# Optimization experiments

Hardware: AMD Instinct MI355X
Metric: run time of the kernel (lower is better)

The kernel has to match this reference:

```python
import jax, jax.numpy as jnp
import numpy as np

EPS = 1e-7          # K.epsilon()
START_TEMP = 10.0
MIN_TEMP = 0.1
ALPHA = 0.99999


def setup_inputs() -> dict:
    key = jax.random.key(0)
    k1, k2, k3, k4 = jax.random.split(key, 4)
    batch, n_feat, bins, out_dim = 4096, 20000, 64, 256
    X = jax.random.normal(k1, (batch, n_feat), dtype=jnp.float32)
    u = jax.random.normal(k2, (n_feat, bins), dtype=jnp.float32)
    # keras 'uniform' initializer ~ U(-0.05, 0.05)
    tinyW = jax.random.uniform(k3, (bins, out_dim), minval=-0.05, maxval=0.05, dtype=jnp.float32)
    uniform = jax.random.uniform(k4, (out_dim, n_feat), minval=EPS, maxval=1.0, dtype=jnp.float32)
    return {"X": X, "u": u, "tinyW": tinyW, "uniform": uniform}


def reference(X, u, tinyW, uniform):
    # al = softmax(u @ tinyW) over output_dim axis, then transpose -> (D, N)
    al = jax.nn.softmax(jnp.dot(u, tinyW), axis=-1).T            # (D, N)
    logits = jnp.log(10.0 * jnp.clip(al, EPS, 0.9999999))        # (D, N)
    gumbel = -jnp.log(-jnp.log(uniform))                          # (D, N)
    temp = jnp.maximum(MIN_TEMP, START_TEMP * ALPHA)              # one K.update step
    samples = jax.nn.softmax((logits + gumbel) / temp, axis=-1)   # (D, N)

    D, N = samples.shape

    # Greedy global-argmax with row/column suppression (inference path).
    # Each of the D iterations picks the global max of p, marks dl[x, y] = 1,
    # then masks row x and column y with -1 (as the numpy loop does).
    def step(carry, _):
        p, dl = carry
        ind = jnp.argmax(p)            # flat argmax over D*N
        x = ind // N
        y = ind % N
        dl = dl.at[x, y].set(1.0)
        p = p.at[x, :].set(-1.0)
        p = p.at[:, y].set(-1.0)
        return (p, dl), None

    (_, dl), _ = jax.lax.scan(step, (samples, jnp.zeros_like(samples)), None, length=D)
    # After D iterations each row of dl has exactly one 1, so
    # one_hot(argmax(dl, axis=-1)) == dl; selections = dl in inference mode.
    Y = jnp.dot(X, dl.T)               # (batch, D)
    return Y
```

## Files before the change

kernel.cpp:

```cpp
#include <hip/hip_runtime.h>
#include <cmath>
#include <cfloat>
#include <climits>

#define NFEAT 20000
#define DDIM 256
#define KDIM 64
#define NSEG 313
#define SEGP 320

__device__ __forceinline__ double z_post(double Lraw, float uu) {
  double L = fmin(fmax(Lraw, -16.118095650958320), -1.0000000500000034e-7);
  double g = -log(-log((double)uu));
  return (2.302585092994045684 + L + g) / 9.9999;
}

__device__ __forceinline__ double compute_z(
    const float* __restrict__ u, const float* __restrict__ W,
    const float* __restrict__ unif, const double* __restrict__ lseN,
    int dd, int n) {
  double acc = 0.0;
  const float* ur = u + (size_t)n * KDIM;
#pragma unroll 8
  for (int k = 0; k < KDIM; ++k)
    acc = fma((double)ur[k], (double)W[k * DDIM + dd], acc);
  double Lraw = acc - lseN[n];
  return z_post(Lraw, unif[(size_t)dd * NFEAT + n]);
}

__global__ __launch_bounds__(256) void k_seg(
    const float* __restrict__ u, const float* __restrict__ W,
    const float* __restrict__ unif, double* __restrict__ lseN,
    double* __restrict__ segVal, double* __restrict__ segSum,
    int* __restrict__ segCol) {
  const int s = blockIdx.x;
  const int n0 = s * 64;
  const int nv = min(64, NFEAT - n0);
  const int d = threadIdx.x;
  const int lane = d & 63, w = d >> 6;

  __shared__ __align__(16) float ut[64 * 64];
  __shared__ float unT[32 * 256];
  __shared__ double ssum[4][8];
  __shared__ double logZs[8];

  for (int i = d; i < 64 * 64; i += 256) {
    int r = i >> 6;
    ut[i] = (r < nv) ? u[(size_t)(n0 + r) * KDIM + (i & 63)] : 0.f;
  }
  float wcol[64];
#pragma unroll
  for (int k = 0; k < KDIM; ++k) wcol[k] = W[k * DDIM + d];

  double ssl = 0.0;
  double segm = -INFINITY;
  int segc = -1;

  for (int half = 0; half < 2; ++half) {
    const int hn0 = half * 32;
    if (hn0 >= nv) break;
    const int hnv = min(32, nv - hn0);
    __syncthreads();
    for (int q = 0; q < hnv; q += 4) {
      const float4 t =
          *(const float4*)(unif + (size_t)d * NFEAT + n0 + hn0 + q);
      unT[(q + 0) * 256 + d] = t.x;
      unT[(q + 1) * 256 + d] = t.y;
      unT[(q + 2) * 256 + d] = t.z;
      unT[(q + 3) * 256 + d] = t.w;
    }
    __syncthreads();

    for (int b0 = hn0; b0 < hn0 + hnv; b0 += 8) {
      double acc[8];
#pragma unroll
      for (int i = 0; i < 8; ++i) acc[i] = 0.0;
#pragma unroll
      for (int k4 = 0; k4 < 16; ++k4) {
        const int kb = k4 * 4;
        const double w0 = (double)wcol[kb + 0], w1 = (double)wcol[kb + 1];
        const double w2 = (double)wcol[kb + 2], w3 = (double)wcol[kb + 3];
#pragma unroll
        for (int i = 0; i < 8; ++i) {
          const float4 uv = *(const float4*)&ut[(b0 + i) * 64 + kb];
          acc[i] = fma((double)uv.x, w0, acc[i]);
          acc[i] = fma((double)uv.y, w1, acc[i]);
          acc[i] = fma((double)uv.z, w2, acc[i]);
          acc[i] = fma((double)uv.w, w3, acc[i]);
        }
      }
      double sl[8];
#pragma unroll
      for (int i = 0; i < 8; ++i) sl[i] = exp(acc[i]);
#pragma unroll
      for (int off = 1; off < 64; off <<= 1)
#pragma unroll
        for (int i = 0; i < 8; ++i) sl[i] += __shfl_xor(sl[i], off, 64);
      if (lane == 0)
#pragma unroll
        for (int i = 0; i < 8; ++i) ssum[w][i] = sl[i];
      __syncthreads();
      if (d < 8) {
        double tot = ssum[0][d] + ssum[1][d] + ssum[2][d] + ssum[3][d];
        double lz = log(tot);
        logZs[d] = lz;
        lseN[n0 + b0 + d] = lz;
      }
      __syncthreads();
#pragma unroll 2
      for (int i = 0; i < 8; ++i) {
        const int n = n0 + b0 + i;
        const double zz =
            z_post(acc[i] - logZs[i], unT[(b0 + i - hn0) * 256 + d]);
        ssl += exp(zz);
        if (zz > segm) { segm = zz; segc = n; }
      }
      __syncthreads();
    }
  }
  segVal[(size_t)d * SEGP + s] = segm;
  segCol[(size_t)d * SEGP + s] = segc;
  segSum[(size_t)d * SEGP + s] = ssl;
}

__global__ __launch_bounds__(64) void k_rowstat(
    const double* __restrict__ segVal, const double* __restrict__ segSum,
    const int* __restrict__ segCol, double* __restrict__ logL,
    double* __restrict__ bestKey, int* __restrict__ bestCol) {
  const int dd = blockIdx.x, lane = threadIdx.x;
  double sum = 0.0, bv = -INFINITY;
  int bc = INT_MAX;
  for (int s = lane; s < NSEG; s += 64) {
    sum += segSum[(size_t)dd * SEGP + s];
    double v = segVal[(size_t)dd * SEGP + s];
    int c = segCol[(size_t)dd * SEGP + s];
    if (c >= 0 && (v > bv || (v == bv && c < bc))) { bv = v; bc = c; }
  }
#pragma unroll
  for (int off = 32; off > 0; off >>= 1) {
    sum += __shfl_xor(sum, off, 64);
    double ov = __shfl_xor(bv, off, 64);
    int oc = __shfl_xor(bc, off, 64);
    if (ov > bv || (ov == bv && oc < bc)) { bv = ov; bc = oc; }
  }
  if (lane == 0) {
    double lL = log(sum);
    logL[dd] = lL;
    bestKey[dd] = bv - lL;
    bestCol[dd] = bc;
  }
}

__global__ __launch_bounds__(64) void k_greedy(
    const float* __restrict__ u, const float* __restrict__ W,
    const float* __restrict__ unif, const double* __restrict__ lseN,
    double* __restrict__ segVal, int* __restrict__ segCol,
    const double* __restrict__ logL, const double* __restrict__ bestKey,
    const int* __restrict__ bestCol, int* __restrict__ sel) {
  const int lane = threadIdx.x;
  __shared__ double kk[DDIM], sk[DDIM];
  __shared__ int sr[DDIM], sc[DDIM], selL[DDIM];
  __shared__ unsigned int supp[NFEAT / 32];
  for (int i = lane; i < NFEAT / 32; i += 64) supp[i] = 0u;

  double myk[4];
  int myc[4];
#pragma unroll
  for (int i = 0; i < 4; ++i) {
    int dd = lane + 64 * i;
    myk[i] = bestKey[dd];
    myc[i] = bestCol[dd];
    kk[dd] = myk[i];
  }
  __syncthreads();
#pragma unroll
  for (int i = 0; i < 4; ++i) {
    int dd = lane + 64 * i;
    int rk = 0;
#pragma unroll 4
    for (int j = 0; j < DDIM; ++j) {
      double kj = kk[j];
      if (kj > myk[i] || (kj == myk[i] && j < dd)) ++rk;
    }
    sk[rk] = myk[i];
    sr[rk] = dd;
    sc[rk] = myc[i];
  }
  __syncthreads();

  int pos = 0;
  while (pos < DDIM) {
    const int p = pos + lane;
    const bool valid = p < DDIM;
    double kcur = 0.0;
    int r = -1, c = -1000000 - lane;
    if (valid) { kcur = sk[p]; r = sr[p]; c = sc[p]; }
    bool conf = !valid;
    if (valid) conf = (supp[c >> 5] >> (c & 31)) & 1u;
    bool dup = false;
#pragma unroll
    for (int j = 0; j < 63; ++j) {
      int cj = __shfl(c, j, 64);
      if (j < lane && cj == c) dup = true;
    }
    if (valid && dup) conf = true;
    unsigned long long bm = __ballot(conf);
    int fc = bm ? (__ffsll(bm) - 1) : 64;
    if (lane < fc) {
      selL[r] = c;
      atomicOr(&supp[c >> 5], 1u << (c & 31));
    }
    __syncthreads();
    pos += fc;
    if (fc < 64 && pos < DDIM) {
      const int rr = sr[pos];
      double pbv = -INFINITY;
      int pbc = INT_MAX;
      int stale[5];
      int scnt = 0;
#pragma unroll
      for (int i2 = 0; i2 < 5; ++i2) {
        int s2 = lane + 64 * i2;
        if (s2 < NSEG) {
          double v = segVal[(size_t)rr * SEGP + s2];
          int cc = segCol[(size_t)rr * SEGP + s2];
          if (cc >= 0) {
            if ((supp[cc >> 5] >> (cc & 31)) & 1u) stale[scnt++] = s2;
            else if (v > pbv || (v == pbv && cc < pbc)) { pbv = v; pbc = cc; }
          }
        }
      }
      unsigned long long sm2 = __ballot(scnt > 0);
      while (sm2) {
        int src = __ffsll(sm2) - 1;
        int cand = (scnt > 0) ? stale[scnt - 1] : 0;
        int s2 = __shfl(cand, src, 64);
        if (lane == src) --scnt;
        int ccol = s2 * 64 + lane;
        double zv = -INFINITY;
        if (ccol < NFEAT && !((supp[ccol >> 5] >> (ccol & 31)) & 1u))
          zv = compute_z(u, W, unif, lseN, rr, ccol);
        int zc = (zv == -INFINITY) ? INT_MAX : ccol;
#pragma unroll
        for (int off = 32; off > 0; off >>= 1) {
          double ov = __shfl_xor(zv, off, 64);
          int oc = __shfl_xor(zc, off, 64);
          if (ov > zv || (ov == zv && oc < zc)) { zv = ov; zc = oc; }
        }
        if (lane == 0) {
          segVal[(size_t)rr * SEGP + s2] = (zc == INT_MAX) ? -INFINITY : zv;
          segCol[(size_t)rr * SEGP + s2] = (zc == INT_MAX) ? -1 : zc;
        }
        if (zc != INT_MAX && (zv > pbv || (zv == pbv && zc < pbc))) {
          pbv = zv;
          pbc = zc;
        }
        sm2 = __ballot(scnt > 0);
      }
#pragma unroll
      for (int off = 32; off > 0; off >>= 1) {
        double ov = __shfl_xor(pbv, off, 64);
        int oc = __shfl_xor(pbc, off, 64);
        if (ov > pbv || (ov == pbv && oc < pbc)) { pbv = ov; pbc = oc; }
      }
      const double knew = pbv - logL[rr];
      const int cn = pbc;
      int cnt = 0;
      for (int q = pos + 1 + lane; q < DDIM; q += 64) {
        double kq = sk[q];
        int rq = sr[q];
        if (kq > knew || (kq == knew && rq < rr)) ++cnt;
      }
#pragma unroll
      for (int off = 32; off > 0; off >>= 1) cnt += __shfl_xor(cnt, off, 64);
      for (int q0 = pos + 1; q0 <= pos + cnt; q0 += 64) {
        int q = q0 + lane;
        double tk = 0.0;
        int tr = 0, tc = 0;
        bool v2 = q <= pos + cnt;
        if (v2) { tk = sk[q]; tr = sr[q]; tc = sc[q]; }
        __syncthreads();
        if (v2) { sk[q - 1] = tk; sr[q - 1] = tr; sc[q - 1] = tc; }
        __syncthreads();
      }
      if (lane == 0) { sk[pos + cnt] = knew; sr[pos + cnt] = rr; sc[pos + cnt] = cn; }
      __syncthreads();
    }
  }
#pragma unroll
  for (int i = 0; i < 4; ++i) sel[lane + 64 * i] = selL[lane + 64 * i];
}

__global__ __launch_bounds__(256) void k_gather(const float* __restrict__ X,
                                                float* out) {
  const int dd = threadIdx.x;
  const size_t b = (size_t)blockIdx.x + 1;
  const int y = __float_as_int(out[dd]);
  out[b * DDIM + dd] = X[b * NFEAT + y];
}

__global__ __launch_bounds__(256) void k_row0(const float* __restrict__ X,
                                              float* out) {
  const int dd = threadIdx.x;
  const int y = __float_as_int(out[dd]);
  const float v = X[y];
  out[dd] = v;
}

extern "C" void kernel_launch(void* const* d_in, const int* in_sizes, int n_in,
                              void* d_out, int out_size, void* d_ws,
                              size_t ws_size, hipStream_t stream) {
  (void)in_sizes; (void)n_in; (void)d_ws; (void)ws_size; (void)out_size;
  const float* X = (const float*)d_in[0];
  const float* u = (const float*)d_in[1];
  const float* W = (const float*)d_in[2];
  const float* unif = (const float*)d_in[3];

  char* ob = (char*)d_out;
  int* sel = (int*)ob;
  double* lseN = (double*)(ob + 1024);
  double* logL = (double*)(ob + 161024);
  double* bestKey = (double*)(ob + 163072);
  int* bestCol = (int*)(ob + 165120);
  double* segVal = (double*)(ob + 166144);
  double* segSum = (double*)(ob + 821504);
  int* segCol = (int*)(ob + 1476864);

  k_seg<<<NSEG, 256, 0, stream>>>(u, W, unif, lseN, segVal, segSum, segCol);
  k_rowstat<<<DDIM, 64, 0, stream>>>(segVal, segSum, segCol, logL, bestKey,
                                     bestCol);
  k_greedy<<<1, 64, 0, stream>>>(u, W, unif, lseN, segVal, segCol, logL,
                                 bestKey, bestCol, sel);
  k_gather<<<4095, 256, 0, stream>>>(X, (float*)d_out);
  k_row0<<<1, 256, 0, stream>>>(X, (float*)d_out);
}
```

Before: 669.2 us.

## Switch to log2 domain with custom exp2/log2 and halve segment size

Moves the score computation into base-2 logarithms, using hand-written double-precision polynomial exp2 and log2 in place of the library exp and log. It also pre-scales u by log2(e) in shared memory as doubles. Segments shrink from 64 to 32 columns, so there are twice as many blocks in k_seg and finer-grained stale-segment recomputation in the greedy pass. This targets transcendental cost and low occupancy (313 blocks), at the risk of tiny numerical differences that could change argmax tie-breaking, and larger per-row scans in the greedy kernel.

```diff
diff --git a/kernel.cpp b/kernel.cpp
--- a/kernel.cpp
+++ b/kernel.cpp
@@ -6,16 +6,61 @@
 #define NFEAT 20000
 #define DDIM 256
 #define KDIM 64
-#define NSEG 313
-#define SEGP 320
-
-__device__ __forceinline__ double z_post(double Lraw, float uu) {
-  double L = fmin(fmax(Lraw, -16.118095650958320), -1.0000000500000034e-7);
-  double g = -log(-log((double)uu));
-  return (2.302585092994045684 + L + g) / 9.9999;
-}
-
-__device__ __forceinline__ double compute_z(
+#define SEGN 32
+#define NSEG 625
+#define SEGP 640
+
+#define LOG2E 1.4426950408889634
+#define INVT (1.0 / 9.9999)
+#define LOG2_10 3.3219280948873623
+#define G2C 0.5287663729448976
+#define LO2 -23.253496664211536
+#define HI2 -1.4426951130237154e-7
+
+__device__ __forceinline__ double fexp2(double x) {
+  const double nd = rint(x);
+  const double y = (x - nd) * 0.6931471805599453;
+  double p = 1.0 / 3628800.0;
+  p = fma(p, y, 1.0 / 362880.0);
+  p = fma(p, y, 1.0 / 40320.0);
+  p = fma(p, y, 1.0 / 5040.0);
+  p = fma(p, y, 1.0 / 720.0);
+  p = fma(p, y, 1.0 / 120.0);
+  p = fma(p, y, 1.0 / 24.0);
+  p = fma(p, y, 1.0 / 6.0);
+  p = fma(p, y, 0.5);
+  p = fma(p, y, 1.0);
+  p = fma(p, y, 1.0);
+  const int n = (int)nd;
+  const double sc = __longlong_as_double((long long)(n + 1023) << 52);
+  return p * sc;
+}
+
+__device__ __forceinline__ double flog2(double x) {
+  const long long b = __double_as_longlong(x);
+  int e = (int)(b >> 52) - 1023;
+  double m = __longlong_as_double((b & 0xfffffffffffffLL) | 0x3ff0000000000000LL);
+  if (m > 1.4142135623730951) { m *= 0.5; e += 1; }
+  const double t = (m - 1.0) / (m + 1.0);
+  const double w = t * t;
+  double p = 1.0 / 13.0;
+  p = fma(p, w, 1.0 / 11.0);
+  p = fma(p, w, 1.0 / 9.0);
+  p = fma(p, w, 1.0 / 7.0);
+  p = fma(p, w, 1.0 / 5.0);
+  p = fma(p, w, 1.0 / 3.0);
+  p = fma(p, w, 1.0);
+  return fma((2.0 * LOG2E) * t, p, (double)e);
+}
+
+__device__ __forceinline__ double z2_post(double L2raw, float uu) {
+  const double L2 = fmin(fmax(L2raw, LO2), HI2);
+  const double t = -flog2((double)uu);
+  const double g2 = G2C - flog2(t);
+  return (LOG2_10 + L2 + g2) * INVT;
+}
+
+__device__ __forceinline__ double compute_z2(
     const float* __restrict__ u, const float* __restrict__ W,
     const float* __restrict__ unif, const double* __restrict__ lseN,
     int dd, int n) {
@@ -23,9 +68,8 @@
   const float* ur = u + (size_t)n * KDIM;
 #pragma unroll 8
   for (int k = 0; k < KDIM; ++k)
-    acc = fma((double)ur[k], (double)W[k * DDIM + dd], acc);
-  double Lraw = acc - lseN[n];
-  return z_post(Lraw, unif[(size_t)dd * NFEAT + n]);
+    acc = fma((double)ur[k] * LOG2E, (double)W[k * DDIM + dd], acc);
+  return z2_post(acc - lseN[n], unif[(size_t)dd * NFEAT + n]);
 }
 
 __global__ __launch_bounds__(256) void k_seg(
@@ -34,89 +78,78 @@
     double* __restrict__ segVal, double* __restrict__ segSum,
     int* __restrict__ segCol) {
   const int s = blockIdx.x;
-  const int n0 = s * 64;
-  const int nv = min(64, NFEAT - n0);
+  const int n0 = s * SEGN;
   const int d = threadIdx.x;
   const int lane = d & 63, w = d >> 6;
 
-  __shared__ __align__(16) float ut[64 * 64];
-  __shared__ float unT[32 * 256];
+  __shared__ __align__(16) double ut2[SEGN][KDIM];
+  __shared__ float unT[SEGN][DDIM];
   __shared__ double ssum[4][8];
-  __shared__ double logZs[8];
-
-  for (int i = d; i < 64 * 64; i += 256) {
-    int r = i >> 6;
-    ut[i] = (r < nv) ? u[(size_t)(n0 + r) * KDIM + (i & 63)] : 0.f;
-  }
-  float wcol[64];
+  __shared__ double lse2s[8];
+
+  for (int i = d; i < SEGN * KDIM; i += 256)
+    ut2[i >> 6][i & 63] =
+        (double)u[(size_t)(n0 + (i >> 6)) * KDIM + (i & 63)] * LOG2E;
+  for (int q = 0; q < SEGN; q += 4) {
+    const float4 t = *(const float4*)(unif + (size_t)d * NFEAT + n0 + q);
+    unT[q + 0][d] = t.x;
+    unT[q + 1][d] = t.y;
+    unT[q + 2][d] = t.z;
+    unT[q + 3][d] = t.w;
+  }
+  float wcol[KDIM];
 #pragma unroll
   for (int k = 0; k < KDIM; ++k) wcol[k] = W[k * DDIM + d];
+  __syncthreads();
 
   double ssl = 0.0;
   double segm = -INFINITY;
   int segc = -1;
 
-  for (int half = 0; half < 2; ++half) {
-    const int hn0 = half * 32;
-    if (hn0 >= nv) break;
-    const int hnv = min(32, nv - hn0);
+  for (int b0 = 0; b0 < SEGN; b0 += 8) {
+    double acc[8];
+#pragma unroll
+    for (int i = 0; i < 8; ++i) acc[i] = 0.0;
+#pragma unroll
+    for (int k4 = 0; k4 < 16; ++k4) {
+      const int kb = k4 * 4;
+      const double w0 = (double)wcol[kb + 0], w1 = (double)wcol[kb + 1];
+      const double w2 = (double)wcol[kb + 2], w3 = (double)wcol[kb + 3];
+#pragma unroll
+      for (int i = 0; i < 8; ++i) {
+        const double2 ua = *(const double2*)&ut2[b0 + i][kb];
+        const double2 ub = *(const double2*)&ut2[b0 + i][kb + 2];
+        acc[i] = fma(ua.x, w0, acc[i]);
+        acc[i] = fma(ua.y, w1, acc[i]);
+        acc[i] = fma(ub.x, w2, acc[i]);
+        acc[i] = fma(ub.y, w3, acc[i]);
+      }
+    }
+    double sl[8];
+#pragma unroll
+    for (int i = 0; i < 8; ++i) sl[i] = fexp2(acc[i]);
+#pragma unroll
+    for (int off = 1; off < 64; off <<= 1)
+#pragma unroll
+      for (int i = 0; i < 8; ++i) sl[i] += __shfl_xor(sl[i], off, 64);
+    if (lane == 0)
+#pragma unroll
+      for (int i = 0; i < 8; ++i) ssum[w][i] = sl[i];
     __syncthreads();
-    for (int q = 0; q < hnv; q += 4) {
-      const float4 t =
-          *(const float4*)(unif + (size_t)d * NFEAT + n0 + hn0 + q);
-      unT[(q + 0) * 256 + d] = t.x;
-      unT[(q + 1) * 256 + d] = t.y;
-      unT[(q + 2) * 256 + d] = t.z;
-      unT[(q + 3) * 256 + d] = t.w;
+    if (d < 8) {
+      const double tot = ssum[0][d] + ssum[1][d] + ssum[2][d] + ssum[3][d];
+      const double lz = flog2(tot);
+      lse2s[d] = lz;
+      lseN[n0 + b0 + d] = lz;
     }
     __syncthreads();
-
-    for (int b0 = hn0; b0 < hn0 + hnv; b0 += 8) {
-      double acc[8];
-#pragma unroll
-      for (int i = 0; i < 8; ++i) acc[i] = 0.0;
-#pragma unroll
-      for (int k4 = 0; k4 < 16; ++k4) {
-        const int kb = k4 * 4;
-        const double w0 = (double)wcol[kb + 0], w1 = (double)wcol[kb + 1];
-        const double w2 = (double)wcol[kb + 2], w3 = (double)wcol[kb + 3];
-#pragma unroll
-        for (int i = 0; i < 8; ++i) {
-          const float4 uv = *(const float4*)&ut[(b0 + i) * 64 + kb];
-          acc[i] = fma((double)uv.x, w0, acc[i]);
-          acc[i] = fma((double)uv.y, w1, acc[i]);
-          acc[i] = fma((double)uv.z, w2, acc[i]);
-          acc[i] = fma((double)uv.w, w3, acc[i]);
-        }
-      }
-      double sl[8];
-#pragma unroll
-      for (int i = 0; i < 8; ++i) sl[i] = exp(acc[i]);
-#pragma unroll
-      for (int off = 1; off < 64; off <<= 1)
-#pragma unroll
-        for (int i = 0; i < 8; ++i) sl[i] += __shfl_xor(sl[i], off, 64);
-      if (lane == 0)
-#pragma unroll
-        for (int i = 0; i < 8; ++i) ssum[w][i] = sl[i];
-      __syncthreads();
-      if (d < 8) {
-        double tot = ssum[0][d] + ssum[1][d] + ssum[2][d] + ssum[3][d];
-        double lz = log(tot);
-        logZs[d] = lz;
-        lseN[n0 + b0 + d] = lz;
-      }
-      __syncthreads();
 #pragma unroll 2
-      for (int i = 0; i < 8; ++i) {
-        const int n = n0 + b0 + i;
-        const double zz =
-            z_post(acc[i] - logZs[i], unT[(b0 + i - hn0) * 256 + d]);
-        ssl += exp(zz);
-        if (zz > segm) { segm = zz; segc = n; }
-      }
-      __syncthreads();
-    }
+    for (int i = 0; i < 8; ++i) {
+      const double z2 = z2_post(acc[i] - lse2s[i], unT[b0 + i][d]);
+      ssl += fexp2(z2);
+      if (z2 > segm) { segm = z2; segc = n0 + b0 + i; }
+    }
+    __syncthreads();
   }
   segVal[(size_t)d * SEGP + s] = segm;
   segCol[(size_t)d * SEGP + s] = segc;
@@ -144,7 +177,7 @@
     if (ov > bv || (ov == bv && oc < bc)) { bv = ov; bc = oc; }
   }
   if (lane == 0) {
-    double lL = log(sum);
+    double lL = flog2(sum);
     logL[dd] = lL;
     bestKey[dd] = bv - lL;
     bestCol[dd] = bc;
@@ -189,12 +222,11 @@
   __syncthreads();
 
   int pos = 0;
-  while (pos < DDIM) {
+  for (int guard = 0; guard < 4 * DDIM && pos < DDIM; ++guard) {
     const int p = pos + lane;
     const bool valid = p < DDIM;
-    double kcur = 0.0;
     int r = -1, c = -1000000 - lane;
-    if (valid) { kcur = sk[p]; r = sr[p]; c = sc[p]; }
+    if (valid) { r = sr[p]; c = sc[p]; }
     bool conf = !valid;
     if (valid) conf = (supp[c >> 5] >> (c & 31)) & 1u;
     bool dup = false;
@@ -216,10 +248,10 @@
       const int rr = sr[pos];
       double pbv = -INFINITY;
       int pbc = INT_MAX;
-      int stale[5];
+      int stale[10];
       int scnt = 0;
 #pragma unroll
-      for (int i2 = 0; i2 < 5; ++i2) {
+      for (int i2 = 0; i2 < 10; ++i2) {
         int s2 = lane + 64 * i2;
         if (s2 < NSEG) {
           double v = segVal[(size_t)rr * SEGP + s2];
@@ -231,15 +263,15 @@
         }
       }
       unsigned long long sm2 = __ballot(scnt > 0);
-      while (sm2) {
+      for (int g2 = 0; g2 < NSEG + 4 && sm2; ++g2) {
         int src = __ffsll(sm2) - 1;
         int cand = (scnt > 0) ? stale[scnt - 1] : 0;
         int s2 = __shfl(cand, src, 64);
         if (lane == src) --scnt;
-        int ccol = s2 * 64 + lane;
+        int ccol = s2 * SEGN + lane;
         double zv = -INFINITY;
-        if (ccol < NFEAT && !((supp[ccol >> 5] >> (ccol & 31)) & 1u))
-          zv = compute_z(u, W, unif, lseN, rr, ccol);
+        if (lane < SEGN && !((supp[ccol >> 5] >> (ccol & 31)) & 1u))
+          zv = compute_z2(u, W, unif, lseN, rr, ccol);
         int zc = (zv == -INFINITY) ? INT_MAX : ccol;
 #pragma unroll
         for (int off = 32; off > 0; off >>= 1) {
@@ -323,8 +355,8 @@
   double* bestKey = (double*)(ob + 163072);
   int* bestCol = (int*)(ob + 165120);
   double* segVal = (double*)(ob + 166144);
-  double* segSum = (double*)(ob + 821504);
-  int* segCol = (int*)(ob + 1476864);
+  double* segSum = (double*)(ob + 1476864);
+  int* segCol = (int*)(ob + 2787584);
 
   k_seg<<<NSEG, 256, 0, stream>>>(u, W, unif, lseN, segVal, segSum, segCol);
   k_rowstat<<<DDIM, 64, 0, stream>>>(segVal, segSum, segCol, logL, bestKey,
```

After: 633.7 us. 5.3% less time.
